# Kernel tuning notes

Measured on AMD Instinct MI355X. Metric: run time of the kernel, lower is better.

Reference implementation:

```python
import jax, jax.numpy as jnp
import numpy as np

B, S, EMB, H = 4, 1024, 1024, 16
HD = EMB // H          # head_dim = 64
MAXP = 512             # RelativePositionalEncoder default max_position


def setup_inputs() -> dict:
    key = jax.random.key(0)
    ks = jax.random.split(key, 13)
    s = 1.0 / np.sqrt(EMB)  # xavier-ish scale keeps softmax logits sane
    return {
        "query": jax.random.normal(ks[0], (B, S, EMB), jnp.float32),
        "key": jax.random.normal(ks[1], (B, S, EMB), jnp.float32),
        "value": jax.random.normal(ks[2], (B, S, EMB), jnp.float32),
        "Wq": jax.random.normal(ks[3], (EMB, EMB), jnp.float32) * s,
        "bq": jnp.zeros((EMB,), jnp.float32),
        "Wk": jax.random.normal(ks[4], (EMB, EMB), jnp.float32) * s,
        "bk": jnp.zeros((EMB,), jnp.float32),
        "Wv": jax.random.normal(ks[5], (EMB, EMB), jnp.float32) * s,
        "bv": jnp.zeros((EMB,), jnp.float32),
        "Wo": jax.random.normal(ks[6], (EMB, EMB), jnp.float32) * s,
        "bo": jnp.zeros((EMB,), jnp.float32),
        "rel_k": jax.random.normal(ks[7], (2 * MAXP + 1, HD), jnp.float32) * 0.05,
        "rel_v": jax.random.normal(ks[8], (2 * MAXP + 1, HD), jnp.float32) * 0.05,
    }


def _split_heads(x):
    # [B,S,E] -> [B,S,H,HD] -> [B,H,S,HD] -> [B*H,S,HD]
    return x.reshape(B, S, H, HD).transpose(0, 2, 1, 3).reshape(B * H, S, HD)


def reference(query, key, value, Wq, bq, Wk, bk, Wv, bv, Wo, bo, rel_k, rel_v):
    scale = jnp.sqrt(jnp.asarray(HD, query.dtype))
    q = _split_heads(query @ Wq + bq)
    k = _split_heads(key @ Wk + bk)
    v = _split_heads(value @ Wv + bv)
    # relative position lookup tables: [Sq, Sk, HD]
    rp = jnp.clip(jnp.arange(S)[None, :] - jnp.arange(S)[:, None], -MAXP, MAXP) + MAXP
    a_key = rel_k[rp]
    a_value = rel_v[rp]
    qk = jnp.einsum('bqd,bkd->bqk', q, k)              # [B*H,S,S]
    rel_qk = jnp.einsum('bqd,qkd->bqk', q, a_key)      # relative score term
    attn = jax.nn.softmax((qk + rel_qk) / scale, axis=-1)
    out = jnp.einsum('bqk,bkd->bqd', attn, v) + jnp.einsum('bqk,qkd->bqd', attn, a_value)
    # faithful to original's view(num_heads, batch, -1, head_dim) then concat reshape
    out = out.reshape(H, B, S, HD).transpose(0, 2, 1, 3).reshape(B, S, H * HD)
    out = out @ Wo + bo
    return (out, attn)
```

## Files before the change

### kernel.cpp

```cpp
#include <hip/hip_runtime.h>


using s16x8 = __attribute__((ext_vector_type(8))) short;
using f32x4 = __attribute__((ext_vector_type(4))) float;

#define MFMA16 __builtin_amdgcn_mfma_f32_16x16x32_bf16

__device__ __forceinline__ float bf2f(unsigned short u) {
  union { unsigned int u; float f; } v; v.u = ((unsigned int)u) << 16; return v.f;
}
__device__ __forceinline__ unsigned short f2bf(float f) {
  union { float f; unsigned int u; } v; v.f = f;
  unsigned int r = (v.u + 0x7FFFu + ((v.u >> 16) & 1u)) >> 16;
  return (unsigned short)r;
}

__global__ __launch_bounds__(256)
void k_prep(const float* __restrict__ Wq, const float* __restrict__ Wk,
            const float* __restrict__ Wv, const float* __restrict__ Wo,
            unsigned short* __restrict__ wqt, unsigned short* __restrict__ wkt,
            unsigned short* __restrict__ wvt, unsigned short* __restrict__ wot,
            const float* __restrict__ rk, const float* __restrict__ rv,
            unsigned short* __restrict__ relkb, unsigned short* __restrict__ rvTb) {
  const int b = blockIdx.x;
  const int tid = threadIdx.x;
  if (b < 4096) {
    __shared__ float t[32][33];
    const int sel = b >> 10, idx = b & 1023;
    const float* W = sel == 0 ? Wq : (sel == 1 ? Wk : (sel == 2 ? Wv : Wo));
    unsigned short* Wt = sel == 0 ? wqt : (sel == 1 ? wkt : (sel == 2 ? wvt : wot));
    const int n0 = (idx & 31) * 32, k0 = (idx >> 5) * 32;
    const int tx = tid & 31, ty = tid >> 5;
#pragma unroll
    for (int r = 0; r < 4; ++r)
      t[ty * 4 + r][tx] = W[(size_t)(k0 + ty * 4 + r) * 1024 + n0 + tx];
    __syncthreads();
#pragma unroll
    for (int r = 0; r < 4; ++r)
      Wt[(size_t)(n0 + ty * 4 + r) * 1024 + k0 + tx] = f2bf(t[tx][ty * 4 + r]);
  } else {
    const int b2 = b - 4096;
    if (b2 < 33) {
      int i = (b2 * 256 + tid) * 8;
      if (i < 65600) {
        float4 a = *(const float4*)(rk + i);
        float4 c = *(const float4*)(rk + i + 4);
        s16x8 o;
        o[0] = (short)f2bf(a.x); o[1] = (short)f2bf(a.y); o[2] = (short)f2bf(a.z); o[3] = (short)f2bf(a.w);
        o[4] = (short)f2bf(c.x); o[5] = (short)f2bf(c.y); o[6] = (short)f2bf(c.z); o[7] = (short)f2bf(c.w);
        *(s16x8*)(relkb + i) = o;
      }
    } else {
      int i = (b2 - 33) * 256 + tid;
      if (i < 65600) {
        int p = i >> 6, d = i & 63;
        rvTb[d * 1040 + p] = f2bf(rv[i]);
      }
    }
  }
}

__global__ __launch_bounds__(256)
void k_trV(const unsigned short* __restrict__ v, unsigned short* __restrict__ vt) {
  __shared__ unsigned short T[64][72];
  const int tid = threadIdx.x;
  const int bh = blockIdx.x >> 4;
  const int s0 = (blockIdx.x & 15) << 6;
  const int r = tid >> 2, cb = (tid & 3) << 4;
  const unsigned short* src = v + ((size_t)bh << 16) + (size_t)(s0 + r) * 64 + cb;
  *(s16x8*)&T[r][cb] = *(const s16x8*)src;
  *(s16x8*)&T[r][cb + 8] = *(const s16x8*)(src + 8);
  __syncthreads();
  unsigned short* dst = vt + ((size_t)bh << 16) + (size_t)r * 1024 + s0 + cb;
  s16x8 o0, o1;
#pragma unroll
  for (int e = 0; e < 8; ++e) o0[e] = T[cb + e][r];
#pragma unroll
  for (int e = 0; e < 8; ++e) o1[e] = T[cb + 8 + e][r];
  *(s16x8*)dst = o0;
  *(s16x8*)(dst + 8) = o1;
}

__global__ __launch_bounds__(256, 2)
void k_gemm_qkv(const float* __restrict__ Aq, const float* __restrict__ Ak, const float* __restrict__ Av,
                const unsigned short* __restrict__ Wq_, const unsigned short* __restrict__ Wk_,
                const unsigned short* __restrict__ Wv_,
                const float* __restrict__ bq_, const float* __restrict__ bk_, const float* __restrict__ bv_,
                unsigned short* __restrict__ Oq, unsigned short* __restrict__ Ok,
                unsigned short* __restrict__ Ov) {
  const int z = blockIdx.z;
  const float* A = z == 0 ? Aq : (z == 1 ? Ak : Av);
  const unsigned short* BT = z == 0 ? Wq_ : (z == 1 ? Wk_ : Wv_);
  const float* bias = z == 0 ? bq_ : (z == 1 ? bk_ : bv_);
  unsigned short* Cout = z == 0 ? Oq : (z == 1 ? Ok : Ov);

  __shared__ alignas(16) unsigned short aT[2][4096];
  __shared__ alignas(16) unsigned short bT[2][2048];
  const int tid = threadIdx.x;
  const int lane = tid & 63;
  const int l15 = lane & 15, lhi = lane >> 4;
  const int w = tid >> 6;
  const int wr = w * 32;
  const int brow = blockIdx.y * 128, bcol = blockIdx.x * 64;
  f32x4 acc[2][4] = {};

  const int c1 = tid, c2 = tid + 256;
  const int r1 = c1 >> 2, kA1 = (c1 & 3) * 8;
  const int r2 = c2 >> 2, kA2 = (c2 & 3) * 8;
  float4 a0, a1, a2, a3;
  s16x8 w1v, w2v;

#define LOADA(kt) do {                                                     \
    const float* p1 = A + (size_t)(brow + r1) * 1024 + (kt) * 32 + kA1;    \
    a0 = *(const float4*)p1; a1 = *(const float4*)(p1 + 4);                \
    const float* p2 = A + (size_t)(brow + r2) * 1024 + (kt) * 32 + kA2;    \
    a2 = *(const float4*)p2; a3 = *(const float4*)(p2 + 4);                \
  } while (0)
#define CVTA() do {                                                        \
    w1v[0] = (short)f2bf(a0.x); w1v[1] = (short)f2bf(a0.y);                \
    w1v[2] = (short)f2bf(a0.z); w1v[3] = (short)f2bf(a0.w);                \
    w1v[4] = (short)f2bf(a1.x); w1v[5] = (short)f2bf(a1.y);                \
    w1v[6] = (short)f2bf(a1.z); w1v[7] = (short)f2bf(a1.w);                \
    w2v[0] = (short)f2bf(a2.x); w2v[1] = (short)f2bf(a2.y);                \
    w2v[2] = (short)f2bf(a2.z); w2v[3] = (short)f2bf(a2.w);                \
    w2v[4] = (short)f2bf(a3.x); w2v[5] = (short)f2bf(a3.y);                \
    w2v[6] = (short)f2bf(a3.z); w2v[7] = (short)f2bf(a3.w);                \
  } while (0)
#define WRA(buf) do {                                                      \
    *(s16x8*)&aT[buf][c1 * 8] = w1v;                                       \
    *(s16x8*)&aT[buf][c2 * 8] = w2v;                                       \
  } while (0)
#define GLB(buf, kt) do {                                                  \
    int row = c1 >> 2, k8 = (c1 & 3) * 8;                                  \
    __builtin_amdgcn_global_load_lds(                                      \
      (const __attribute__((address_space(1))) void*)(BT + (size_t)(bcol + row) * 1024 + (kt) * 32 + k8), \
      (__attribute__((address_space(3))) void*)(&bT[buf][c1 * 8]), 16, 0, 0); \
  } while (0)

  LOADA(0); GLB(0, 0); CVTA(); WRA(0);
  int cur = 0;
  for (int kt = 0; kt < 32; ++kt) {
    __syncthreads();
    if (kt + 1 < 32) { LOADA(kt + 1); GLB(cur ^ 1, kt + 1); }
    s16x8 af[2], bfv[4];
#pragma unroll
    for (int m = 0; m < 2; ++m)
      af[m] = *(const s16x8*)&aT[cur][(wr + m * 16 + l15) * 32 + lhi * 8];
#pragma unroll
    for (int n = 0; n < 4; ++n)
      bfv[n] = *(const s16x8*)&bT[cur][(n * 16 + l15) * 32 + lhi * 8];
#pragma unroll
    for (int m = 0; m < 2; ++m)
#pragma unroll
      for (int n = 0; n < 4; ++n)
        acc[m][n] = MFMA16(af[m], bfv[n], acc[m][n], 0, 0, 0);
    if (kt + 1 < 32) { CVTA(); WRA(cur ^ 1); }
    __syncthreads();
    cur ^= 1;
  }
#undef LOADA
#undef CVTA
#undef WRA
#undef GLB

#pragma unroll
  for (int m = 0; m < 2; ++m) {
#pragma unroll
    for (int n = 0; n < 4; ++n) {
      int col = bcol + n * 16 + l15;
      float bs = bias[col];
#pragma unroll
      for (int j = 0; j < 4; ++j) {
        int r = brow + wr + m * 16 + lhi * 4 + j;
        float v = acc[m][n][j] + bs;
        int bb = r >> 10, s = r & 1023, h = col >> 6, d = col & 63;
        Cout[(((size_t)((bb << 4) + h) * 1024 + s) << 6) + d] = f2bf(v);
      }
    }
  }
}

__global__ __launch_bounds__(256, 2)
void k_gemm_o(const unsigned short* __restrict__ A, const unsigned short* __restrict__ BT,
              const float* __restrict__ bias, float* __restrict__ Cout) {
  __shared__ alignas(16) unsigned short aT[2][4096];
  __shared__ alignas(16) unsigned short bT[2][2048];
  const int tid = threadIdx.x;
  const int lane = tid & 63;
  const int l15 = lane & 15, lhi = lane >> 4;
  const int w = tid >> 6;
  const int wr = w * 32;
  const int brow = blockIdx.y * 128, bcol = blockIdx.x * 64;
  f32x4 acc[2][4] = {};

#define STAGE(buf, kt) do {                                                              \
    int k0s = (kt) * 32;                                                                 \
    {                                                                                    \
      int c = tid;                                                                       \
      int row = c >> 2, k8 = (c & 3) * 8;                                                \
      __builtin_amdgcn_global_load_lds(                                                  \
        (const __attribute__((address_space(1))) void*)(A + (size_t)(brow + row) * 1024 + k0s + k8), \
        (__attribute__((address_space(3))) void*)(&aT[buf][c * 8]), 16, 0, 0);           \
      __builtin_amdgcn_global_load_lds(                                                  \
        (const __attribute__((address_space(1))) void*)(BT + (size_t)(bcol + row) * 1024 + k0s + k8),\
        (__attribute__((address_space(3))) void*)(&bT[buf][c * 8]), 16, 0, 0);           \
    }                                                                                    \
    {                                                                                    \
      int c = tid + 256;                                                                 \
      int row = c >> 2, k8 = (c & 3) * 8;                                                \
      __builtin_amdgcn_global_load_lds(                                                  \
        (const __attribute__((address_space(1))) void*)(A + (size_t)(brow + row) * 1024 + k0s + k8), \
        (__attribute__((address_space(3))) void*)(&aT[buf][c * 8]), 16, 0, 0);           \
    }                                                                                    \
  } while (0)

  int cur = 0;
  STAGE(0, 0);
  for (int kt = 0; kt < 32; ++kt) {
    __syncthreads();
    if (kt + 1 < 32) STAGE(cur ^ 1, kt + 1);
    s16x8 af[2], bfv[4];
#pragma unroll
    for (int m = 0; m < 2; ++m)
      af[m] = *(const s16x8*)&aT[cur][(wr + m * 16 + l15) * 32 + lhi * 8];
#pragma unroll
    for (int n = 0; n < 4; ++n)
      bfv[n] = *(const s16x8*)&bT[cur][(n * 16 + l15) * 32 + lhi * 8];
#pragma unroll
    for (int m = 0; m < 2; ++m)
#pragma unroll
      for (int n = 0; n < 4; ++n)
        acc[m][n] = MFMA16(af[m], bfv[n], acc[m][n], 0, 0, 0);
    __syncthreads();
    cur ^= 1;
  }
#undef STAGE

#pragma unroll
  for (int m = 0; m < 2; ++m) {
#pragma unroll
    for (int n = 0; n < 4; ++n) {
      int col = bcol + n * 16 + l15;
      float bs = bias[col];
#pragma unroll
      for (int j = 0; j < 4; ++j) {
        int r = brow + wr + m * 16 + lhi * 4 + j;
        Cout[(size_t)r * 1024 + col] = acc[m][n][j] + bs;
      }
    }
  }
}

#define RPW 1032
#define PWP 520

__global__ __launch_bounds__(256, 3)
void k_attn(const unsigned short* __restrict__ qb, const unsigned short* __restrict__ kbm,
            const unsigned short* __restrict__ vT, const unsigned short* __restrict__ relk,
            const unsigned short* __restrict__ rvT, float* __restrict__ attn_out,
            unsigned short* __restrict__ xscr) {
  __shared__ alignas(16) unsigned short pbuf[16 * RPW];
  __shared__ alignas(16) unsigned short TbPw[16 * PWP];
  __shared__ float red[4][16];
  __shared__ float izS[16], plS[16], phS[16];

  const int tid = threadIdx.x;
  const int lane = tid & 63;
  const int w = tid >> 6;
  const int l15 = lane & 15, lhi = lane >> 4;
  const int orig = ((blockIdx.x & 7) << 9) | (blockIdx.x >> 3);
  const int bh = orig >> 6;
  const int q0 = (orig & 63) << 4;

  const unsigned short* Qh = qb + ((size_t)bh << 16);
  const unsigned short* Kh = kbm + ((size_t)bh << 16);
  const unsigned short* Vth = vT + ((size_t)bh << 16);

  const unsigned short* qp = Qh + (size_t)(q0 + l15) * 64 + lhi * 8;
  s16x8 qa0 = *(const s16x8*)qp;
  s16x8 qa1 = *(const s16x8*)(qp + 32);

  float zp = 0.f;
  for (int half = 0; half < 2; ++half) {
    const int khalf = half << 9;
    __syncthreads();

    {
      const int PT0 = ((khalf - q0 + 497) >> 4) << 4;
      const int PT1 = khalf - q0 + 1023;
      for (int pt = PT0 + w * 16; pt <= PT1; pt += 64) {
        int pr = pt + l15; pr = pr < 0 ? 0 : (pr > 1024 ? 1024 : pr);
        const unsigned short* rp = relk + (size_t)pr * 64 + lhi * 8;
        s16x8 rf0 = *(const s16x8*)rp;
        s16x8 rf1 = *(const s16x8*)(rp + 32);
        f32x4 d = {0.f, 0.f, 0.f, 0.f};
        d = MFMA16(qa0, rf0, d, 0, 0, 0);
        d = MFMA16(qa1, rf1, d, 0, 0, 0);
#pragma unroll
        for (int j = 0; j < 4; ++j) {
          int qi = lhi * 4 + j;
          int u = pt + l15 - khalf + q0 + qi - 512;
          if (u >= 0 && u < 512) TbPw[qi * PWP + u] = f2bf(d[j]);
        }
      }
    }
    __syncthreads();

    const unsigned short* kbp = Kh + (size_t)(khalf + w * 16 + l15) * 64 + lhi * 8;
#pragma unroll
    for (int g = 0; g < 2; ++g) {
      s16x8 kf0[4], kf1[4];
#pragma unroll
      for (int n = 0; n < 4; ++n) {
        const unsigned short* p = kbp + (size_t)(g * 4 + n) * 4096;
        kf0[n] = *(const s16x8*)p;
        kf1[n] = *(const s16x8*)(p + 32);
      }
#pragma unroll
      for (int n = 0; n < 4; ++n) {
        const int ktile = khalf + w * 16 + (g * 4 + n) * 64;
        f32x4 c = {0.f, 0.f, 0.f, 0.f};
        __builtin_amdgcn_s_setprio(1);
        c = MFMA16(kf0[n], qa0, c, 0, 0, 0);
        c = MFMA16(kf1[n], qa1, c, 0, 0, 0);
        __builtin_amdgcn_s_setprio(0);
        uint2 tv = *(const uint2*)&TbPw[l15 * PWP + (ktile - khalf) + lhi * 4];
        float t0 = bf2f((unsigned short)(tv.x & 0xFFFF));
        float t1 = bf2f((unsigned short)(tv.x >> 16));
        float t2 = bf2f((unsigned short)(tv.y & 0xFFFF));
        float t3 = bf2f((unsigned short)(tv.y >> 16));
        float e0 = __expf((c[0] + t0) * 0.125f);
        float e1 = __expf((c[1] + t1) * 0.125f);
        float e2 = __expf((c[2] + t2) * 0.125f);
        float e3 = __expf((c[3] + t3) * 0.125f);
        zp += (e0 + e1) + (e2 + e3);
        uint2 pk;
        pk.x = (unsigned int)f2bf(e0) | ((unsigned int)f2bf(e1) << 16);
        pk.y = (unsigned int)f2bf(e2) | ((unsigned int)f2bf(e3) << 16);
        *(uint2*)&pbuf[l15 * RPW + ktile + lhi * 4] = pk;
      }
    }
  }

  zp += __shfl_xor(zp, 16, 64);
  zp += __shfl_xor(zp, 32, 64);
  if (lane < 16) red[w][lane] = zp;
  __syncthreads();
  if (tid < 16)
    izS[tid] = 1.0f / (red[0][tid] + red[1][tid] + red[2][tid] + red[3][tid]);

  {
    const int qi = tid >> 4, tq = tid & 15;
    const int qa = q0 + qi;
    int lo, hi;
    const bool isPh = (qa < 512);
    if (isPh) { lo = qa + 512; hi = 1024; }
    else      { lo = 0;        hi = qa - 511; }
    float s = 0.f;
    const unsigned short* srow = pbuf + qi * RPW;
    const int kb0 = lo & ~7;
    for (int k8 = kb0 + tq * 8; k8 < hi; k8 += 128) {
      s16x8 v8 = *(const s16x8*)&srow[k8];
#pragma unroll
      for (int e = 0; e < 8; ++e) {
        int k = k8 + e;
        s += (k >= lo && k < hi) ? bf2f((unsigned short)v8[e]) : 0.f;
      }
    }
#pragma unroll
    for (int off = 1; off < 16; off <<= 1) s += __shfl_xor(s, off, 64);
    if (tq == 0) { plS[qi] = isPh ? 0.f : s; phS[qi] = isPh ? s : 0.f; }
  }

  const int sqi = tid >> 4, stq = tid & 15;
  const int ssh = sqi & 7, shs = ssh >> 1;
  const bool sodd = (ssh & 1) != 0;
  unsigned short* drow = TbPw + sqi * PWP;
  const unsigned short* srowp = pbuf + sqi * RPW;

#define STAGE_PW(base, doSlot0) do {                                         \
    for (int t = stq; t < 64; t += 16) {                                     \
      const int kw0 = (base) + t * 8;                                        \
      s16x8 o;                                                               \
      if (kw0 >= 0 && kw0 + 8 <= 1024) {                                     \
        const int A = kw0 - ssh;                                             \
        union { s16x8 v; unsigned int u[4]; } a0u, a1u, ov;                  \
        a0u.v = *(const s16x8*)&srowp[A];                                    \
        a1u.v = *(const s16x8*)&srowp[A + 8];                                \
        unsigned int wd[8];                                                  \
        _Pragma("unroll")                                                    \
        for (int j2 = 0; j2 < 4; ++j2) { wd[j2] = a0u.u[j2]; wd[4 + j2] = a1u.u[j2]; } \
        unsigned int v7[7];                                                  \
        _Pragma("unroll")                                                    \
        for (int j2 = 0; j2 < 7; ++j2) {                                     \
          unsigned int sf = (wd[j2] >> 16) | (wd[j2 + 1] << 16);             \
          v7[j2] = sodd ? sf : wd[j2];                                       \
        }                                                                    \
        _Pragma("unroll")                                                    \
        for (int j2 = 0; j2 < 4; ++j2) {                                     \
          unsigned int t0 = (shs & 1) ? v7[j2 + 1] : v7[j2];                 \
          unsigned int t1 = (shs & 1) ? v7[j2 + 3] : v7[j2 + 2];             \
          ov.u[j2] = (shs & 2) ? t1 : t0;                                    \
        }                                                                    \
        o = ov.v;                                                            \
      } else if (kw0 + 8 <= 0 || kw0 >= 1024) {                              \
        o = (s16x8){0, 0, 0, 0, 0, 0, 0, 0};                                 \
      } else {                                                               \
        _Pragma("unroll")                                                    \
        for (int e = 0; e < 8; ++e) {                                        \
          int k = kw0 + e;                                                   \
          int kc2 = k < 0 ? 0 : (k > 1023 ? 1023 : k);                       \
          unsigned short vv = srowp[kc2];                                    \
          o[e] = (k >= 0 && k < 1024) ? (short)vv : (short)0;                \
        }                                                                    \
      }                                                                      \
      *(s16x8*)&drow[t * 8] = o;                                             \
      if ((doSlot0) && t == 0) drow[0] = f2bf(plS[sqi]);                     \
    }                                                                        \
  } while (0)

  STAGE_PW(q0 + sqi - 512, true);

  f32x4 acc = {0.f, 0.f, 0.f, 0.f};
  const int d0w = w << 4;
  const unsigned short* vrow = Vth + (size_t)(d0w + l15) * 1024 + lhi * 8;
#pragma unroll 8
  for (int kc = 0; kc < 1024; kc += 32) {
    s16x8 pa = *(const s16x8*)&pbuf[l15 * RPW + kc + lhi * 8];
    s16x8 vf = *(const s16x8*)(vrow + kc);
    acc = MFMA16(pa, vf, acc, 0, 0, 0);
  }

  __syncthreads();

  {
    float* ao = attn_out + ((size_t)bh << 20) + ((size_t)q0 << 10);
#pragma unroll
    for (int n = 0; n < 8; ++n) {
      int row = (tid >> 7) + n * 2;
      int c8 = (tid & 127) << 3;
      float iz = izS[row];
      s16x8 p8 = *(const s16x8*)&pbuf[row * RPW + c8];
      f32x4 o0, o1;
      o0[0] = bf2f((unsigned short)p8[0]) * iz; o0[1] = bf2f((unsigned short)p8[1]) * iz;
      o0[2] = bf2f((unsigned short)p8[2]) * iz; o0[3] = bf2f((unsigned short)p8[3]) * iz;
      o1[0] = bf2f((unsigned short)p8[4]) * iz; o1[1] = bf2f((unsigned short)p8[5]) * iz;
      o1[2] = bf2f((unsigned short)p8[6]) * iz; o1[3] = bf2f((unsigned short)p8[7]) * iz;
      __builtin_nontemporal_store(o0, (f32x4*)(ao + (row << 10) + c8));
      __builtin_nontemporal_store(o1, (f32x4*)(ao + (row << 10) + c8 + 4));
    }
  }

  const unsigned short* rrow = rvT + (size_t)(d0w + l15) * 1040 + lhi * 8;
#pragma unroll 8
  for (int kc = 0; kc < 512; kc += 32) {
    s16x8 pa = *(const s16x8*)&TbPw[l15 * PWP + kc + lhi * 8];
    s16x8 rb = *(const s16x8*)(rrow + kc);
    acc = MFMA16(pa, rb, acc, 0, 0, 0);
  }

  __syncthreads();
  STAGE_PW(q0 + sqi, false);
  __syncthreads();

#pragma unroll 8
  for (int kc = 0; kc < 512; kc += 32) {
    s16x8 pa = *(const s16x8*)&TbPw[l15 * PWP + kc + lhi * 8];
    s16x8 rb = *(const s16x8*)(rrow + 512 + kc);
    acc = MFMA16(pa, rb, acc, 0, 0, 0);
  }
#undef STAGE_PW

  float rv1024 = bf2f(rvT[(size_t)(d0w + l15) * 1040 + 1024]);
  const size_t fb = ((size_t)(bh >> 2) << 18) + ((size_t)(bh & 3) << 6);
#pragma unroll
  for (int j = 0; j < 4; ++j) {
    int qi = lhi * 4 + j;
    float v = (acc[j] + phS[qi] * rv1024) * izS[qi];
    xscr[fb + ((size_t)(q0 + qi) << 8) + d0w + l15] = f2bf(v);
  }
}

extern "C" void kernel_launch(void* const* d_in, const int* in_sizes, int n_in,
                              void* d_out, int out_size, void* d_ws, size_t ws_size,
                              hipStream_t stream) {
  (void)in_sizes; (void)n_in; (void)out_size; (void)ws_size;
  const float* query = (const float*)d_in[0];
  const float* key   = (const float*)d_in[1];
  const float* value = (const float*)d_in[2];
  const float* Wq = (const float*)d_in[3];
  const float* bq = (const float*)d_in[4];
  const float* Wk = (const float*)d_in[5];
  const float* bk = (const float*)d_in[6];
  const float* Wv = (const float*)d_in[7];
  const float* bv = (const float*)d_in[8];
  const float* Wo = (const float*)d_in[9];
  const float* bo = (const float*)d_in[10];
  const float* rel_k = (const float*)d_in[11];
  const float* rel_v = (const float*)d_in[12];

  char* ws = (char*)d_ws;
  const size_t MB = 1024 * 1024;
  unsigned short* qb    = (unsigned short*)(ws);
  unsigned short* kbuf  = (unsigned short*)(ws + 8 * MB);
  unsigned short* vbuf  = (unsigned short*)(ws + 16 * MB);
  unsigned short* vTb   = (unsigned short*)(ws + 24 * MB);
  unsigned short* wqt   = (unsigned short*)(ws + 32 * MB);
  unsigned short* wkt   = (unsigned short*)(ws + 34 * MB);
  unsigned short* wvt   = (unsigned short*)(ws + 36 * MB);
  unsigned short* wot   = (unsigned short*)(ws + 38 * MB);
  unsigned short* relkb = (unsigned short*)(ws + 40 * MB);
  unsigned short* rvTb  = (unsigned short*)(ws + 40 * MB + 256 * 1024);
  unsigned short* xscr  = vbuf;

  float* out0 = (float*)d_out;
  float* attn_out = out0 + 4194304;

  k_prep<<<4386, 256, 0, stream>>>(Wq, Wk, Wv, Wo, wqt, wkt, wvt, wot,
                                   rel_k, rel_v, relkb, rvTb);

  k_gemm_qkv<<<dim3(16, 32, 3), 256, 0, stream>>>(query, key, value,
                                                  wqt, wkt, wvt,
                                                  bq, bk, bv,
                                                  qb, kbuf, vbuf);

  k_trV<<<1024, 256, 0, stream>>>(vbuf, vTb);

  k_attn<<<4096, 256, 0, stream>>>(qb, kbuf, vTb, relkb, rvTb, attn_out, xscr);

  k_gemm_o<<<dim3(16, 32), 256, 0, stream>>>(xscr, wot, bo, out0);
}
```

Measured before the change: 335.4 us.

## Double attention block to 512 threads and specialize half for attn output stores

The attention kernel now launches 512 threads per block. All eight waves share the score/exp phase, each handling half as many key tiles. Afterward the first 256 threads do the row-sum, rel-value staging and PV MFMAs, while the other 256 write the normalized attention matrix to global memory concurrently. This overlaps the large fp32 attn store with the P·V compute. In exchange it drops the occupancy hint of 3 blocks per CU, which may change register allocation, and leaves half the threads idle during the later rel-value stages.

Result: no change. 334.8 us (-0.2%).

```diff
diff --git a/kernel.cpp b/kernel.cpp
--- a/kernel.cpp
+++ b/kernel.cpp
@@ -254,14 +254,14 @@
 #define RPW 1032
 #define PWP 520
 
-__global__ __launch_bounds__(256, 3)
+__global__ __launch_bounds__(512)
 void k_attn(const unsigned short* __restrict__ qb, const unsigned short* __restrict__ kbm,
             const unsigned short* __restrict__ vT, const unsigned short* __restrict__ relk,
             const unsigned short* __restrict__ rvT, float* __restrict__ attn_out,
             unsigned short* __restrict__ xscr) {
   __shared__ alignas(16) unsigned short pbuf[16 * RPW];
   __shared__ alignas(16) unsigned short TbPw[16 * PWP];
-  __shared__ float red[4][16];
+  __shared__ float red[8][16];
   __shared__ float izS[16], plS[16], phS[16];
 
   const int tid = threadIdx.x;
@@ -288,7 +288,7 @@
     {
       const int PT0 = ((khalf - q0 + 497) >> 4) << 4;
       const int PT1 = khalf - q0 + 1023;
-      for (int pt = PT0 + w * 16; pt <= PT1; pt += 64) {
+      for (int pt = PT0 + w * 16; pt <= PT1; pt += 128) {
         int pr = pt + l15; pr = pr < 0 ? 0 : (pr > 1024 ? 1024 : pr);
         const unsigned short* rp = relk + (size_t)pr * 64 + lhi * 8;
         s16x8 rf0 = *(const s16x8*)rp;
@@ -307,38 +307,35 @@
     __syncthreads();
 
     const unsigned short* kbp = Kh + (size_t)(khalf + w * 16 + l15) * 64 + lhi * 8;
-#pragma unroll
-    for (int g = 0; g < 2; ++g) {
-      s16x8 kf0[4], kf1[4];
-#pragma unroll
-      for (int n = 0; n < 4; ++n) {
-        const unsigned short* p = kbp + (size_t)(g * 4 + n) * 4096;
-        kf0[n] = *(const s16x8*)p;
-        kf1[n] = *(const s16x8*)(p + 32);
-      }
-#pragma unroll
-      for (int n = 0; n < 4; ++n) {
-        const int ktile = khalf + w * 16 + (g * 4 + n) * 64;
-        f32x4 c = {0.f, 0.f, 0.f, 0.f};
-        __builtin_amdgcn_s_setprio(1);
-        c = MFMA16(kf0[n], qa0, c, 0, 0, 0);
-        c = MFMA16(kf1[n], qa1, c, 0, 0, 0);
-        __builtin_amdgcn_s_setprio(0);
-        uint2 tv = *(const uint2*)&TbPw[l15 * PWP + (ktile - khalf) + lhi * 4];
-        float t0 = bf2f((unsigned short)(tv.x & 0xFFFF));
-        float t1 = bf2f((unsigned short)(tv.x >> 16));
-        float t2 = bf2f((unsigned short)(tv.y & 0xFFFF));
-        float t3 = bf2f((unsigned short)(tv.y >> 16));
-        float e0 = __expf((c[0] + t0) * 0.125f);
-        float e1 = __expf((c[1] + t1) * 0.125f);
-        float e2 = __expf((c[2] + t2) * 0.125f);
-        float e3 = __expf((c[3] + t3) * 0.125f);
-        zp += (e0 + e1) + (e2 + e3);
-        uint2 pk;
-        pk.x = (unsigned int)f2bf(e0) | ((unsigned int)f2bf(e1) << 16);
-        pk.y = (unsigned int)f2bf(e2) | ((unsigned int)f2bf(e3) << 16);
-        *(uint2*)&pbuf[l15 * RPW + ktile + lhi * 4] = pk;
-      }
+    s16x8 kf0[4], kf1[4];
+#pragma unroll
+    for (int n = 0; n < 4; ++n) {
+      const unsigned short* p = kbp + (size_t)n * 8192;
+      kf0[n] = *(const s16x8*)p;
+      kf1[n] = *(const s16x8*)(p + 32);
+    }
+#pragma unroll
+    for (int n = 0; n < 4; ++n) {
+      const int ktile = khalf + w * 16 + n * 128;
+      f32x4 c = {0.f, 0.f, 0.f, 0.f};
+      __builtin_amdgcn_s_setprio(1);
+      c = MFMA16(kf0[n], qa0, c, 0, 0, 0);
+      c = MFMA16(kf1[n], qa1, c, 0, 0, 0);
+      __builtin_amdgcn_s_setprio(0);
+      uint2 tv = *(const uint2*)&TbPw[l15 * PWP + (ktile - khalf) + lhi * 4];
+      float t0 = bf2f((unsigned short)(tv.x & 0xFFFF));
+      float t1 = bf2f((unsigned short)(tv.x >> 16));
+      float t2 = bf2f((unsigned short)(tv.y & 0xFFFF));
+      float t3 = bf2f((unsigned short)(tv.y >> 16));
+      float e0 = __expf((c[0] + t0) * 0.125f);
+      float e1 = __expf((c[1] + t1) * 0.125f);
+      float e2 = __expf((c[2] + t2) * 0.125f);
+      float e3 = __expf((c[3] + t3) * 0.125f);
+      zp += (e0 + e1) + (e2 + e3);
+      uint2 pk;
+      pk.x = (unsigned int)f2bf(e0) | ((unsigned int)f2bf(e1) << 16);
+      pk.y = (unsigned int)f2bf(e2) | ((unsigned int)f2bf(e3) << 16);
+      *(uint2*)&pbuf[l15 * RPW + ktile + lhi * 4] = pk;
     }
   }
 
@@ -347,36 +344,18 @@
   if (lane < 16) red[w][lane] = zp;
   __syncthreads();
   if (tid < 16)
-    izS[tid] = 1.0f / (red[0][tid] + red[1][tid] + red[2][tid] + red[3][tid]);
-
-  {
-    const int qi = tid >> 4, tq = tid & 15;
-    const int qa = q0 + qi;
-    int lo, hi;
-    const bool isPh = (qa < 512);
-    if (isPh) { lo = qa + 512; hi = 1024; }
-    else      { lo = 0;        hi = qa - 511; }
-    float s = 0.f;
-    const unsigned short* srow = pbuf + qi * RPW;
-    const int kb0 = lo & ~7;
-    for (int k8 = kb0 + tq * 8; k8 < hi; k8 += 128) {
-      s16x8 v8 = *(const s16x8*)&srow[k8];
-#pragma unroll
-      for (int e = 0; e < 8; ++e) {
-        int k = k8 + e;
-        s += (k >= lo && k < hi) ? bf2f((unsigned short)v8[e]) : 0.f;
-      }
-    }
-#pragma unroll
-    for (int off = 1; off < 16; off <<= 1) s += __shfl_xor(s, off, 64);
-    if (tq == 0) { plS[qi] = isPh ? 0.f : s; phS[qi] = isPh ? s : 0.f; }
-  }
-
-  const int sqi = tid >> 4, stq = tid & 15;
+    izS[tid] = 1.0f / (red[0][tid] + red[1][tid] + red[2][tid] + red[3][tid] +
+                       red[4][tid] + red[5][tid] + red[6][tid] + red[7][tid]);
+
+  f32x4 acc = {0.f, 0.f, 0.f, 0.f};
+  const int d0w = (w & 3) << 4;
+  const int sqi = (tid & 255) >> 4, stq = tid & 15;
   const int ssh = sqi & 7, shs = ssh >> 1;
   const bool sodd = (ssh & 1) != 0;
   unsigned short* drow = TbPw + sqi * PWP;
   const unsigned short* srowp = pbuf + sqi * RPW;
+  const unsigned short* vrow = Vth + (size_t)(d0w + l15) * 1024 + lhi * 8;
+  const unsigned short* rrow = rvT + (size_t)(d0w + l15) * 1040 + lhi * 8;
 
 #define STAGE_PW(base, doSlot0) do {                                         \
     for (int t = stq; t < 64; t += 16) {                                     \
@@ -419,27 +398,48 @@
     }                                                                        \
   } while (0)
 
-  STAGE_PW(q0 + sqi - 512, true);
-
-  f32x4 acc = {0.f, 0.f, 0.f, 0.f};
-  const int d0w = w << 4;
-  const unsigned short* vrow = Vth + (size_t)(d0w + l15) * 1024 + lhi * 8;
+  if (tid < 256) {
+    {
+      const int qi = tid >> 4, tq = tid & 15;
+      const int qa = q0 + qi;
+      int lo, hi;
+      const bool isPh = (qa < 512);
+      if (isPh) { lo = qa + 512; hi = 1024; }
+      else      { lo = 0;        hi = qa - 511; }
+      float s = 0.f;
+      const unsigned short* srow = pbuf + qi * RPW;
+      const int kb0 = lo & ~7;
+      for (int k8 = kb0 + tq * 8; k8 < hi; k8 += 128) {
+        s16x8 v8 = *(const s16x8*)&srow[k8];
+#pragma unroll
+        for (int e = 0; e < 8; ++e) {
+          int k = k8 + e;
+          s += (k >= lo && k < hi) ? bf2f((unsigned short)v8[e]) : 0.f;
+        }
+      }
+#pragma unroll
+      for (int off = 1; off < 16; off <<= 1) s += __shfl_xor(s, off, 64);
+      if (tq == 0) { plS[qi] = isPh ? 0.f : s; phS[qi] = isPh ? s : 0.f; }
+    }
+
+    STAGE_PW(q0 + sqi - 512, true);
+
 #pragma unroll 8
-  for (int kc = 0; kc < 1024; kc += 32) {
-    s16x8 pa = *(const s16x8*)&pbuf[l15 * RPW + kc + lhi * 8];
-    s16x8 vf = *(const s16x8*)(vrow + kc);
-    acc = MFMA16(pa, vf, acc, 0, 0, 0);
-  }
-
-  __syncthreads();
-
-  {
+    for (int kc = 0; kc < 1024; kc += 32) {
+      s16x8 pa = *(const s16x8*)&pbuf[l15 * RPW + kc + lhi * 8];
+      s16x8 vf = *(const s16x8*)(vrow + kc);
+      acc = MFMA16(pa, vf, acc, 0, 0, 0);
+    }
+  } else {
+    const int t2 = tid - 256;
     float* ao = attn_out + ((size_t)bh << 20) + ((size_t)q0 << 10);
 #pragma unroll
     for (int n = 0; n < 8; ++n) {
-      int row = (tid >> 7) + n * 2;
-      int c8 = (tid & 127) << 3;
-      float iz = izS[row];
+      int row = (t2 >> 7) + n * 2;
+      int c8 = (t2 & 127) << 3;
+      float zs = red[0][row] + red[1][row] + red[2][row] + red[3][row] +
+                 red[4][row] + red[5][row] + red[6][row] + red[7][row];
+      float iz = 1.0f / zs;
       s16x8 p8 = *(const s16x8*)&pbuf[row * RPW + c8];
       f32x4 o0, o1;
       o0[0] = bf2f((unsigned short)p8[0]) * iz; o0[1] = bf2f((unsigned short)p8[1]) * iz;
@@ -451,34 +451,37 @@
     }
   }
 
-  const unsigned short* rrow = rvT + (size_t)(d0w + l15) * 1040 + lhi * 8;
+  __syncthreads();
+
+  if (tid < 256) {
 #pragma unroll 8
-  for (int kc = 0; kc < 512; kc += 32) {
-    s16x8 pa = *(const s16x8*)&TbPw[l15 * PWP + kc + lhi * 8];
-    s16x8 rb = *(const s16x8*)(rrow + kc);
-    acc = MFMA16(pa, rb, acc, 0, 0, 0);
-  }
-
+    for (int kc = 0; kc < 512; kc += 32) {
+      s16x8 pa = *(const s16x8*)&TbPw[l15 * PWP + kc + lhi * 8];
+      s16x8 rb = *(const s16x8*)(rrow + kc);
+      acc = MFMA16(pa, rb, acc, 0, 0, 0);
+    }
+  }
   __syncthreads();
-  STAGE_PW(q0 + sqi, false);
+  if (tid < 256) STAGE_PW(q0 + sqi, false);
   __syncthreads();
 
+  if (tid < 256) {
 #pragma unroll 8
-  for (int kc = 0; kc < 512; kc += 32) {
-    s16x8 pa = *(const s16x8*)&TbPw[l15 * PWP + kc + lhi * 8];
-    s16x8 rb = *(const s16x8*)(rrow + 512 + kc);
-    acc = MFMA16(pa, rb, acc, 0, 0, 0);
+    for (int kc = 0; kc < 512; kc += 32) {
+      s16x8 pa = *(const s16x8*)&TbPw[l15 * PWP + kc + lhi * 8];
+      s16x8 rb = *(const s16x8*)(rrow + 512 + kc);
+      acc = MFMA16(pa, rb, acc, 0, 0, 0);
+    }
+    float rv1024 = bf2f(rvT[(size_t)(d0w + l15) * 1040 + 1024]);
+    const size_t fb = ((size_t)(bh >> 2) << 18) + ((size_t)(bh & 3) << 6);
+#pragma unroll
+    for (int j = 0; j < 4; ++j) {
+      int qi = lhi * 4 + j;
+      float v = (acc[j] + phS[qi] * rv1024) * izS[qi];
+      xscr[fb + ((size_t)(q0 + qi) << 8) + d0w + l15] = f2bf(v);
+    }
   }
 #undef STAGE_PW
-
-  float rv1024 = bf2f(rvT[(size_t)(d0w + l15) * 1040 + 1024]);
-  const size_t fb = ((size_t)(bh >> 2) << 18) + ((size_t)(bh & 3) << 6);
-#pragma unroll
-  for (int j = 0; j < 4; ++j) {
-    int qi = lhi * 4 + j;
-    float v = (acc[j] + phS[qi] * rv1024) * izS[qi];
-    xscr[fb + ((size_t)(q0 + qi) << 8) + d0w + l15] = f2bf(v);
-  }
 }
 
 extern "C" void kernel_launch(void* const* d_in, const int* in_sizes, int n_in,
@@ -526,7 +529,7 @@
 
   k_trV<<<1024, 256, 0, stream>>>(vbuf, vTb);
 
-  k_attn<<<4096, 256, 0, stream>>>(qb, kbuf, vTb, relkb, rvTb, attn_out, xscr);
+  k_attn<<<4096, 512, 0, stream>>>(qb, kbuf, vTb, relkb, rvTb, attn_out, xscr);
 
   k_gemm_o<<<dim3(16, 32), 256, 0, stream>>>(xscr, wot, bo, out0);
 }
```
